# Kernel tuning notes

Measured on AMD Instinct MI355X. Metric: run time of the kernel, lower is better.

The kernel has to match this reference:

```python
import jax, jax.numpy as jnp
import numpy as np

N, C, E = 50000, 128, 800000
HEADS, S_TYPES = 4, 3
ATTN_DIM = 128
HEAD_DIM = ATTN_DIM // HEADS
LN_EPS = 1e-5


def setup_inputs() -> dict:
    key = jax.random.key(0)
    ks = jax.random.split(key, 12)
    sc = 1.0 / np.sqrt(C)
    return {
        "x": jax.random.normal(ks[0], (N, C), jnp.float32),
        "structure_type": jax.random.randint(ks[1], (N,), 0, S_TYPES),
        "edge_index": jax.random.randint(ks[2], (2, E), 0, N),
        "Wq": jax.random.normal(ks[3], (C, ATTN_DIM), jnp.float32) * sc,
        "bq": jnp.zeros((ATTN_DIM,), jnp.float32),
        "Wk": jax.random.normal(ks[4], (C, ATTN_DIM), jnp.float32) * sc,
        "bk": jnp.zeros((ATTN_DIM,), jnp.float32),
        "Wv": jax.random.normal(ks[5], (C, ATTN_DIM), jnp.float32) * sc,
        "bv": jnp.zeros((ATTN_DIM,), jnp.float32),
        "structure_bias": jnp.zeros((S_TYPES, HEADS), jnp.float32),
        "Wo": jax.random.normal(ks[6], (ATTN_DIM, C), jnp.float32) * sc,
        "bo": jnp.zeros((C,), jnp.float32),
        "ln_gamma": jnp.ones((C,), jnp.float32),
        "ln_beta": jnp.zeros((C,), jnp.float32),
    }


def reference(x, structure_type, edge_index, Wq, bq, Wk, bk, Wv, bv,
              structure_bias, Wo, bo, ln_gamma, ln_beta):
    residual = x
    q = (x @ Wq + bq).reshape(N, HEADS, HEAD_DIM)
    k = (x @ Wk + bk).reshape(N, HEADS, HEAD_DIM)
    v = (x @ Wv + bv).reshape(N, HEADS, HEAD_DIM)
    src, dst = edge_index[0], edge_index[1]
    # per-edge scores [E, H]
    attn = jnp.sum(q[dst] * k[src], axis=-1) / np.sqrt(HEAD_DIM)
    attn = attn + structure_bias[structure_type[src]]
    # segment softmax over dst
    m = jax.ops.segment_max(attn, dst, num_segments=N)  # [N, H]
    e = jnp.exp(attn - m[dst])
    s = jax.ops.segment_sum(e, dst, num_segments=N)     # [N, H]
    a = e / (s[dst] + 1e-16)
    # scatter-add messages -> [N, H, Hd]
    out = jax.ops.segment_sum(a[..., None] * v[src], dst, num_segments=N)
    out = out.reshape(N, ATTN_DIM) @ Wo + bo
    y = residual + out
    mu = jnp.mean(y, axis=-1, keepdims=True)
    var = jnp.var(y, axis=-1, keepdims=True)
    return (y - mu) / jnp.sqrt(var + LN_EPS) * ln_gamma + ln_beta
```

## Files before the change

### kernel.cpp

```cpp
#include <hip/hip_runtime.h>
#include <hip/hip_bf16.h>
#include <hip/hip_fp8.h>

#define HEADS 4
#define CDIM 128
#define INV_SQRT_HD 0.17677669529663687f
#define BCAP 64
#define KVROW 384
#define NBINS 256
#define BINCAP 6144

using short8  = __attribute__((ext_vector_type(8))) short;
using float4v = __attribute__((ext_vector_type(4))) float;

__device__ __forceinline__ float bflo(unsigned u) { return __uint_as_float(u << 16); }
__device__ __forceinline__ float bfhi(unsigned u) { return __uint_as_float(u & 0xffff0000u); }
__device__ __forceinline__ short bfr(float f) {
    __hip_bfloat16 h = __float2bfloat16(f);
    return *(short*)&h;
}

__global__ __launch_bounds__(256) void wswz_kernel(
    const float* __restrict__ Wq, const float* __restrict__ Wk,
    const float* __restrict__ Wv, const float* __restrict__ Wo,
    unsigned short* __restrict__ wt, int* __restrict__ gcur)
{
    int i = blockIdx.x * 256 + threadIdx.x;
    if (i < NBINS) gcur[i] = 0;
    if (i >= 4 * 16384) return;
    int m = i >> 14, rem = i & 16383;
    int col = rem & 127, k = rem >> 7;
    const float* W = (m == 0) ? Wq : (m == 1) ? Wk : (m == 2) ? Wv : Wo;
    wt[(m << 14) + col * 128 + k] = (unsigned short)bfr(W[k * 128 + col]);
}

__global__ __launch_bounds__(256) void qkv_mfma_kernel(
    const float* __restrict__ x, const unsigned short* __restrict__ wt,
    const float* __restrict__ bq, const float* __restrict__ bk,
    const float* __restrict__ bv,
    float* __restrict__ q,
    unsigned char* __restrict__ kvb,
    int N)
{
    __shared__ unsigned short wl[128 * 136];

    const int t = threadIdx.x;
    const int lane = t & 63;
    const int w = t >> 6;
    const int n = lane & 15, qd = lane >> 4;
    const int rowb = blockIdx.x * 64 + w * 16;

    int arow = rowb + n;
    int arowc = (arow < N) ? arow : (N - 1);
    const float4* x4 = (const float4*)(x + (size_t)arowc * 128);
    short8 afrag[4];
    #pragma unroll
    for (int c = 0; c < 4; ++c) {
        float4 f0 = x4[c * 8 + qd * 2];
        float4 f1 = x4[c * 8 + qd * 2 + 1];
        short8 a;
        a[0] = bfr(f0.x); a[1] = bfr(f0.y); a[2] = bfr(f0.z); a[3] = bfr(f0.w);
        a[4] = bfr(f1.x); a[5] = bfr(f1.y); a[6] = bfr(f1.z); a[7] = bfr(f1.w);
        afrag[c] = a;
    }

    for (int m = 0; m < 3; ++m) {
        __syncthreads();
        const uint4* g4 = (const uint4*)(wt + (m << 14));
        #pragma unroll
        for (int i = 0; i < 8; ++i) {
            int id = t + 256 * i;
            int col = id >> 4, ch = id & 15;
            *(uint4*)&wl[col * 136 + ch * 8] = g4[col * 16 + ch];
        }
        __syncthreads();

        float4v acc[8];
        #pragma unroll
        for (int tt = 0; tt < 8; ++tt) acc[tt] = (float4v){0.f, 0.f, 0.f, 0.f};

        #pragma unroll
        for (int c = 0; c < 4; ++c) {
            #pragma unroll
            for (int tt = 0; tt < 8; ++tt) {
                short8 bfrag = *(const short8*)&wl[(tt * 16 + n) * 136 + c * 32 + qd * 8];
                acc[tt] = __builtin_amdgcn_mfma_f32_16x16x32_bf16(
                    afrag[c], bfrag, acc[tt], 0, 0, 0);
            }
        }

        const float* bptr = (m == 0) ? bq : (m == 1) ? bk : bv;
        #pragma unroll
        for (int tt = 0; tt < 8; ++tt) {
            int gcol = tt * 16 + n;
            float bb = bptr[gcol];
            #pragma unroll
            for (int r = 0; r < 4; ++r) {
                int grow = rowb + qd * 4 + r;
                if (grow < N) {
                    float val = acc[tt][r] + bb;
                    if (m == 0) {
                        q[(size_t)grow * 128 + gcol] = val;
                    } else if (m == 1) {
                        *(unsigned short*)(kvb + (size_t)grow * KVROW + gcol * 2)
                            = (unsigned short)bfr(val);
                    } else {
                        __hip_fp8_e4m3 f8(val);
                        kvb[(size_t)grow * KVROW + 256 + gcol] = f8.__x;
                    }
                }
            }
        }
    }
}

#define BIN_EPB 4096
__global__ __launch_bounds__(1024) void bin_kernel(
    const int* __restrict__ ei, const int* __restrict__ stype,
    int* __restrict__ gcur, uint2* __restrict__ binned, int E)
{
    __shared__ int lcnt[NBINS];
    __shared__ int lbase[NBINS];
    const int t = threadIdx.x;
    const int base = blockIdx.x * BIN_EPB;

    if (t < NBINS) lcnt[t] = 0;
    __syncthreads();

    int mybin[4], myloc[4];
    uint2 myent[4];
    #pragma unroll
    for (int j = 0; j < 4; ++j) {
        int i = base + j * 1024 + t;
        mybin[j] = -1;
        if (i < E) {
            int src = ei[i];
            int dst = ei[E + i];
            int st  = stype[src];
            int bin = dst >> 8;
            mybin[j] = bin;
            myloc[j] = atomicAdd(&lcnt[bin], 1);
            myent[j] = make_uint2((unsigned)(src | (st << 16)), (unsigned)dst);
        }
    }
    __syncthreads();

    if (t < NBINS) lbase[t] = atomicAdd(&gcur[t], lcnt[t]);
    __syncthreads();

    #pragma unroll
    for (int j = 0; j < 4; ++j) {
        if (mybin[j] >= 0) {
            int pos = lbase[mybin[j]] + myloc[j];
            if (pos < BINCAP)
                binned[(size_t)mybin[j] * BINCAP + pos] = myent[j];
        }
    }
}

__global__ __launch_bounds__(1024) void bucket_kernel(
    const uint2* __restrict__ binned, const int* __restrict__ gcur,
    int* __restrict__ buckets, int* __restrict__ cnt, int N)
{
    __shared__ int lcnt[256];
    const int t = threadIdx.x;
    const int bin = blockIdx.x;

    if (t < 256) lcnt[t] = 0;
    __syncthreads();

    int ne = gcur[bin];
    ne = (ne < BINCAP) ? ne : BINCAP;
    const uint2* brow = binned + (size_t)bin * BINCAP;

    for (int i = t; i < ne; i += 1024) {
        uint2 e = brow[i];
        int dst = (int)e.y;
        int pos = atomicAdd(&lcnt[dst & 255], 1);
        if (pos < BCAP) buckets[(size_t)dst * BCAP + pos] = (int)e.x;
    }
    __syncthreads();

    if (t < 256) {
        int dst = bin * 256 + t;
        if (dst < N) {
            int c = lcnt[t];
            cnt[dst] = (c < BCAP) ? c : BCAP;
        }
    }
}

__global__ __launch_bounds__(256) void attn_csr_kernel(
    const float* __restrict__ q,
    const unsigned char* __restrict__ kv,
    const int* __restrict__ cnt, const int* __restrict__ buckets,
    const float* __restrict__ sbias,
    unsigned short* __restrict__ h,
    int N)
{
    int wid = (blockIdx.x * 256 + threadIdx.x) >> 6;
    if (wid >= N) return;
    int lane = threadIdx.x & 63;
    int half = lane >> 5;
    int l = lane & 31;
    int hd = l >> 3;

    float sb0 = sbias[hd];
    float sb1 = sbias[HEADS + hd];
    float sb2 = sbias[2 * HEADS + hd];

    int d = cnt[wid];
    d = (d < BCAP) ? d : BCAP;
    const int* brow = buckets + (size_t)wid * BCAP;

    float4 qv = ((const float4*)q)[(size_t)wid * 32 + l];
    float4 acc = make_float4(0.f, 0.f, 0.f, 0.f);
    float sacc = 0.f;

    for (int i = half; i < d; i += 2) {
        int se  = brow[i];
        int src = se & 0xffff;
        const unsigned char* kp = kv + (size_t)src * KVROW;
        uint2    ku = *(const uint2*)(kp + l * 8);
        unsigned vu = *(const unsigned*)(kp + 256 + l * 4);

        float p = qv.x * bflo(ku.x) + qv.y * bfhi(ku.x)
                + qv.z * bflo(ku.y) + qv.w * bfhi(ku.y);
        p += __shfl_xor(p, 1);
        p += __shfl_xor(p, 2);
        p += __shfl_xor(p, 4);

        int st = se >> 16;
        float bias = (st == 0) ? sb0 : ((st == 1) ? sb1 : sb2);
        float ev = __expf(fmaf(p, INV_SQRT_HD, bias));
        acc.x = fmaf(ev, __builtin_amdgcn_cvt_f32_fp8(vu, 0), acc.x);
        acc.y = fmaf(ev, __builtin_amdgcn_cvt_f32_fp8(vu, 1), acc.y);
        acc.z = fmaf(ev, __builtin_amdgcn_cvt_f32_fp8(vu, 2), acc.z);
        acc.w = fmaf(ev, __builtin_amdgcn_cvt_f32_fp8(vu, 3), acc.w);
        sacc += ev;
    }

    acc.x += __shfl_xor(acc.x, 32);
    acc.y += __shfl_xor(acc.y, 32);
    acc.z += __shfl_xor(acc.z, 32);
    acc.w += __shfl_xor(acc.w, 32);
    sacc  += __shfl_xor(sacc, 32);

    float inv = 1.0f / (sacc + 1e-16f);
    if (half == 0) {
        unsigned short hv[4];
        hv[0] = (unsigned short)bfr(acc.x * inv);
        hv[1] = (unsigned short)bfr(acc.y * inv);
        hv[2] = (unsigned short)bfr(acc.z * inv);
        hv[3] = (unsigned short)bfr(acc.w * inv);
        *(uint2*)(h + (size_t)wid * 128 + l * 4) = *(uint2*)hv;
    }
}

__global__ __launch_bounds__(256) void out_ln_mfma_kernel(
    const unsigned short* __restrict__ hbuf, const unsigned short* __restrict__ wt,
    const float* __restrict__ bo, const float* __restrict__ x,
    const float* __restrict__ gamma, const float* __restrict__ beta,
    float* __restrict__ out, int N)
{
    __shared__ unsigned short wl[128 * 136];

    const int t = threadIdx.x;
    const int lane = t & 63;
    const int w = t >> 6;
    const int n = lane & 15, qd = lane >> 4;
    const int rowb = blockIdx.x * 64 + w * 16;

    const uint4* g4 = (const uint4*)(wt + (3 << 14));
    #pragma unroll
    for (int i = 0; i < 8; ++i) {
        int id = t + 256 * i;
        int col = id >> 4, ch = id & 15;
        *(uint4*)&wl[col * 136 + ch * 8] = g4[col * 16 + ch];
    }

    int arow = rowb + n;
    int arowc = (arow < N) ? arow : (N - 1);
    const unsigned short* hrow = hbuf + (size_t)arowc * 128;
    short8 afrag[4];
    #pragma unroll
    for (int c = 0; c < 4; ++c)
        afrag[c] = *(const short8*)(hrow + c * 32 + qd * 8);
    __syncthreads();

    float4v acc[8];
    #pragma unroll
    for (int tt = 0; tt < 8; ++tt) acc[tt] = (float4v){0.f, 0.f, 0.f, 0.f};

    #pragma unroll
    for (int c = 0; c < 4; ++c) {
        #pragma unroll
        for (int tt = 0; tt < 8; ++tt) {
            short8 bfrag = *(const short8*)&wl[(tt * 16 + n) * 136 + c * 32 + qd * 8];
            acc[tt] = __builtin_amdgcn_mfma_f32_16x16x32_bf16(
                afrag[c], bfrag, acc[tt], 0, 0, 0);
        }
    }

    float bov[8];
    #pragma unroll
    for (int tt = 0; tt < 8; ++tt) bov[tt] = bo[tt * 16 + n];

    float sum[4], sq[4];
    #pragma unroll
    for (int r = 0; r < 4; ++r) {
        int grow = rowb + qd * 4 + r;
        int growc = (grow < N) ? grow : (N - 1);
        const float* xr = x + (size_t)growc * 128;
        float s = 0.f, s2 = 0.f;
        #pragma unroll
        for (int tt = 0; tt < 8; ++tt) {
            float yv = acc[tt][r] + bov[tt] + xr[tt * 16 + n];
            acc[tt][r] = yv;
            s += yv;
            s2 += yv * yv;
        }
        sum[r] = s; sq[r] = s2;
    }
    #pragma unroll
    for (int off = 1; off < 16; off <<= 1) {
        #pragma unroll
        for (int r = 0; r < 4; ++r) {
            sum[r] += __shfl_xor(sum[r], off);
            sq[r]  += __shfl_xor(sq[r], off);
        }
    }

    float gv[8], bv2[8];
    #pragma unroll
    for (int tt = 0; tt < 8; ++tt) { gv[tt] = gamma[tt * 16 + n]; bv2[tt] = beta[tt * 16 + n]; }

    #pragma unroll
    for (int r = 0; r < 4; ++r) {
        int grow = rowb + qd * 4 + r;
        if (grow >= N) continue;
        float mu   = sum[r] * (1.0f / 128.0f);
        float var  = sq[r] * (1.0f / 128.0f) - mu * mu;
        float rstd = rsqrtf(var + 1e-5f);
        float* orow = out + (size_t)grow * 128;
        #pragma unroll
        for (int tt = 0; tt < 8; ++tt)
            orow[tt * 16 + n] = (acc[tt][r] - mu) * rstd * gv[tt] + bv2[tt];
    }
}

extern "C" void kernel_launch(void* const* d_in, const int* in_sizes, int n_in,
                              void* d_out, int out_size, void* d_ws, size_t ws_size,
                              hipStream_t stream) {
    const float* x     = (const float*)d_in[0];
    const int*   stype = (const int*)  d_in[1];
    const int*   ei    = (const int*)  d_in[2];
    const float* Wq    = (const float*)d_in[3];
    const float* bq    = (const float*)d_in[4];
    const float* Wk    = (const float*)d_in[5];
    const float* bk    = (const float*)d_in[6];
    const float* Wv    = (const float*)d_in[7];
    const float* bv    = (const float*)d_in[8];
    const float* sbias = (const float*)d_in[9];
    const float* Wo    = (const float*)d_in[10];
    const float* bo    = (const float*)d_in[11];
    const float* gam   = (const float*)d_in[12];
    const float* bet   = (const float*)d_in[13];
    float* out = (float*)d_out;

    const int N = in_sizes[0] / CDIM;
    const int E = in_sizes[2] / 2;

    char* wsb = (char*)d_ws;
    float*          q       = (float*)wsb;
    unsigned short* h       = (unsigned short*)(wsb + (size_t)N * 512);
    unsigned char*  kvb     = (unsigned char*)(wsb + (size_t)N * 768);
    int*            buckets = (int*)(wsb + (size_t)N * 1152);
    int*            cnt     = (int*)(wsb + (size_t)N * 1408);
    size_t gcur_off = (size_t)N * 1408 + (((size_t)N * 4 + 255) & ~(size_t)255);
    int*            gcur    = (int*)(wsb + gcur_off);
    uint2*          binned  = (uint2*)(wsb + gcur_off + 1024);
    unsigned short* wt      = (unsigned short*)(wsb + gcur_off + 1024
                                  + (size_t)NBINS * BINCAP * 8);

    dim3 blk(256);

    wswz_kernel<<<dim3(256), blk, 0, stream>>>(Wq, Wk, Wv, Wo, wt, gcur);

    qkv_mfma_kernel<<<dim3((N + 63) / 64), blk, 0, stream>>>(
        x, wt, bq, bk, bv, q, kvb, N);

    bin_kernel<<<dim3((E + BIN_EPB - 1) / BIN_EPB), dim3(1024), 0, stream>>>(
        ei, stype, gcur, binned, E);

    bucket_kernel<<<dim3(NBINS), dim3(1024), 0, stream>>>(
        binned, gcur, buckets, cnt, N);

    attn_csr_kernel<<<dim3((N * 64 + 255) / 256), blk, 0, stream>>>(
        q, kvb, cnt, buckets, sbias, h, N);

    out_ln_mfma_kernel<<<dim3((N + 63) / 64), blk, 0, stream>>>(
        h, wt, bo, x, gam, bet, out, N);
}
```

Before: 228.9 us.

## Process four edges per wave with wider loads and software-prefetched gathers

The attention gather kernel now splits each 64-lane wave into four 16-lane groups instead of two 32-lane halves. Each lane loads 16 bytes of K and 8 bytes of V per edge, the bucket row is loaded once and distributed with shuffles, and the next edge's K/V gather is issued before the current edge is computed. This is meant to raise memory-level parallelism and cut per-edge load instructions on the latency-bound random gather. In exchange it uses more registers, does extra cross-group reductions at the end, and spends wasted work on masked tail edges. Nodes with no edges now take an early exit that writes zeros.

```diff
diff --git a/kernel.cpp b/kernel.cpp
--- a/kernel.cpp
+++ b/kernel.cpp
@@ -201,9 +201,9 @@
     int wid = (blockIdx.x * 256 + threadIdx.x) >> 6;
     if (wid >= N) return;
     int lane = threadIdx.x & 63;
-    int half = lane >> 5;
-    int l = lane & 31;
-    int hd = l >> 3;
+    int qt = lane >> 4;
+    int ql = lane & 15;
+    int hd = ql >> 2;
 
     float sb0 = sbias[hd];
     float sb1 = sbias[HEADS + hd];
@@ -213,47 +213,87 @@
     d = (d < BCAP) ? d : BCAP;
     const int* brow = buckets + (size_t)wid * BCAP;
 
-    float4 qv = ((const float4*)q)[(size_t)wid * 32 + l];
-    float4 acc = make_float4(0.f, 0.f, 0.f, 0.f);
+    const float4* q4 = (const float4*)(q + (size_t)wid * 128);
+    float4 qa = q4[ql * 2];
+    float4 qb = q4[ql * 2 + 1];
+
+    if (d == 0) {
+        if (qt == 0) {
+            uint4 z = make_uint4(0, 0, 0, 0);
+            *(uint4*)(h + (size_t)wid * 128 + ql * 8) = z;
+        }
+        return;
+    }
+
+    int ent = brow[lane];
+
+    float acc[8] = {0.f, 0.f, 0.f, 0.f, 0.f, 0.f, 0.f, 0.f};
     float sacc = 0.f;
 
-    for (int i = half; i < d; i += 2) {
-        int se  = brow[i];
-        int src = se & 0xffff;
-        const unsigned char* kp = kv + (size_t)src * KVROW;
-        uint2    ku = *(const uint2*)(kp + l * 8);
-        unsigned vu = *(const unsigned*)(kp + 256 + l * 4);
-
-        float p = qv.x * bflo(ku.x) + qv.y * bfhi(ku.x)
-                + qv.z * bflo(ku.y) + qv.w * bfhi(ku.y);
+    int nit = (d + 3) >> 2;
+    int i = qt;
+    int idx0 = (i < d) ? i : (d - 1);
+    int se_c = __shfl(ent, idx0);
+    const unsigned char* kp0 = kv + (size_t)(se_c & 0xffff) * KVROW;
+    uint4 ku_c = *(const uint4*)(kp0 + ql * 16);
+    uint2 vu_c = *(const uint2*)(kp0 + 256 + ql * 8);
+
+    for (int it = 0; it < nit; ++it) {
+        int inext = i + 4;
+        int se_n = se_c;
+        uint4 ku_n = ku_c;
+        uint2 vu_n = vu_c;
+        if (it + 1 < nit) {
+            int idn = (inext < d) ? inext : (d - 1);
+            se_n = __shfl(ent, idn);
+            const unsigned char* kp2 = kv + (size_t)(se_n & 0xffff) * KVROW;
+            ku_n = *(const uint4*)(kp2 + ql * 16);
+            vu_n = *(const uint2*)(kp2 + 256 + ql * 8);
+        }
+
+        float p = qa.x * bflo(ku_c.x) + qa.y * bfhi(ku_c.x)
+                + qa.z * bflo(ku_c.y) + qa.w * bfhi(ku_c.y)
+                + qb.x * bflo(ku_c.z) + qb.y * bfhi(ku_c.z)
+                + qb.z * bflo(ku_c.w) + qb.w * bfhi(ku_c.w);
         p += __shfl_xor(p, 1);
         p += __shfl_xor(p, 2);
-        p += __shfl_xor(p, 4);
-
-        int st = se >> 16;
+
+        int st = se_c >> 16;
         float bias = (st == 0) ? sb0 : ((st == 1) ? sb1 : sb2);
         float ev = __expf(fmaf(p, INV_SQRT_HD, bias));
-        acc.x = fmaf(ev, __builtin_amdgcn_cvt_f32_fp8(vu, 0), acc.x);
-        acc.y = fmaf(ev, __builtin_amdgcn_cvt_f32_fp8(vu, 1), acc.y);
-        acc.z = fmaf(ev, __builtin_amdgcn_cvt_f32_fp8(vu, 2), acc.z);
-        acc.w = fmaf(ev, __builtin_amdgcn_cvt_f32_fp8(vu, 3), acc.w);
+        ev = (i < d) ? ev : 0.f;
+
+        acc[0] = fmaf(ev, __builtin_amdgcn_cvt_f32_fp8(vu_c.x, 0), acc[0]);
+        acc[1] = fmaf(ev, __builtin_amdgcn_cvt_f32_fp8(vu_c.x, 1), acc[1]);
+        acc[2] = fmaf(ev, __builtin_amdgcn_cvt_f32_fp8(vu_c.x, 2), acc[2]);
+        acc[3] = fmaf(ev, __builtin_amdgcn_cvt_f32_fp8(vu_c.x, 3), acc[3]);
+        acc[4] = fmaf(ev, __builtin_amdgcn_cvt_f32_fp8(vu_c.y, 0), acc[4]);
+        acc[5] = fmaf(ev, __builtin_amdgcn_cvt_f32_fp8(vu_c.y, 1), acc[5]);
+        acc[6] = fmaf(ev, __builtin_amdgcn_cvt_f32_fp8(vu_c.y, 2), acc[6]);
+        acc[7] = fmaf(ev, __builtin_amdgcn_cvt_f32_fp8(vu_c.y, 3), acc[7]);
         sacc += ev;
-    }
-
-    acc.x += __shfl_xor(acc.x, 32);
-    acc.y += __shfl_xor(acc.y, 32);
-    acc.z += __shfl_xor(acc.z, 32);
-    acc.w += __shfl_xor(acc.w, 32);
-    sacc  += __shfl_xor(sacc, 32);
-
-    float inv = 1.0f / (sacc + 1e-16f);
-    if (half == 0) {
-        unsigned short hv[4];
-        hv[0] = (unsigned short)bfr(acc.x * inv);
-        hv[1] = (unsigned short)bfr(acc.y * inv);
-        hv[2] = (unsigned short)bfr(acc.z * inv);
-        hv[3] = (unsigned short)bfr(acc.w * inv);
-        *(uint2*)(h + (size_t)wid * 128 + l * 4) = *(uint2*)hv;
+
+        se_c = se_n; ku_c = ku_n; vu_c = vu_n; i = inext;
+    }
+
+    #pragma unroll
+    for (int j = 0; j < 8; ++j) {
+        acc[j] += __shfl_xor(acc[j], 16);
+        acc[j] += __shfl_xor(acc[j], 32);
+    }
+    sacc += __shfl_xor(sacc, 16);
+    sacc += __shfl_xor(sacc, 32);
+
+    if (qt == 0) {
+        float inv = 1.0f / (sacc + 1e-16f);
+        unsigned hw[4];
+        #pragma unroll
+        for (int j = 0; j < 4; ++j) {
+            unsigned lo = (unsigned)(unsigned short)bfr(acc[2 * j] * inv);
+            unsigned hi = (unsigned)(unsigned short)bfr(acc[2 * j + 1] * inv);
+            hw[j] = lo | (hi << 16);
+        }
+        *(uint4*)(h + (size_t)wid * 128 + ql * 8) = *(uint4*)hw;
     }
 }
 
```

Result: faster. 213.4 us (-6.8%).
